# Kernel tuning notes

Measured on AMD Instinct MI355X. Metric: run time of the kernel, lower is better.

Reference implementation:

```python
import jax, jax.numpy as jnp
import numpy as np

N, E = 50000, 800000
IN_DIM, H, OUT = 16, 256, 64
L = 3
REL_DIM, ROLE_DIM, COL_DIM = 16, 8, 8
NUM_REL, NUM_ROLE, NUM_COL = 8, 8, 3
EDGE_IN = 2 * H + REL_DIM + 2 * ROLE_DIM + 2 * COL_DIM   # 560
NODE_IN = 2 * H + ROLE_DIM + COL_DIM                     # 528
LN_EPS = 1e-5


def setup_inputs() -> dict:
    key = jax.random.key(0)
    ks = jax.random.split(key, 32)
    s = 0.02
    inp = {
        "scalars": jax.random.normal(ks[0], (N, IN_DIM), jnp.float32),
        "edge_index": jax.random.randint(ks[1], (2, E), 0, N),
        "edge_relation": jax.random.randint(ks[2], (E,), 0, NUM_REL),
        "node_color_rep": jax.random.randint(ks[3], (N,), 0, NUM_COL),
        "node_role": jax.random.randint(ks[4], (N,), 0, NUM_ROLE),
        # block-level embeddings + input projection (weights stored [in,out])
        "blk_role_emb": jax.random.normal(ks[5], (NUM_ROLE, 8), jnp.float32) * s,
        "blk_color_emb": jax.random.normal(ks[6], (NUM_COL, 8), jnp.float32) * s,
        "in_w": jax.random.normal(ks[7], (IN_DIM + 16, H), jnp.float32) * s,
        "in_b": jnp.zeros((H,), jnp.float32),
        # per-layer params, stacked over L
        "rel_embs": jax.random.normal(ks[8], (L, NUM_REL, REL_DIM), jnp.float32) * s,
        "role_embs": jax.random.normal(ks[9], (L, NUM_ROLE, ROLE_DIM), jnp.float32) * s,
        "col_embs": jax.random.normal(ks[10], (L, NUM_COL, COL_DIM), jnp.float32) * s,
        "e1_w": jax.random.normal(ks[11], (L, EDGE_IN, H), jnp.float32) * s,
        "e1_b": jnp.zeros((L, H), jnp.float32),
        "e2_w": jax.random.normal(ks[12], (L, H, H), jnp.float32) * s,
        "e2_b": jnp.zeros((L, H), jnp.float32),
        "n1_w": jax.random.normal(ks[13], (L, NODE_IN, H), jnp.float32) * s,
        "n1_b": jnp.zeros((L, H), jnp.float32),
        "n2_w": jax.random.normal(ks[14], (L, H, H), jnp.float32) * s,
        "n2_b": jnp.zeros((L, H), jnp.float32),
        "ln_g": jnp.ones((L, H), jnp.float32),
        "ln_b": jnp.zeros((L, H), jnp.float32),
        "out_w": jax.random.normal(ks[15], (H, OUT), jnp.float32) * s,
        "out_b": jnp.zeros((OUT,), jnp.float32),
    }
    return inp


def _layer(h, edge_index, edge_relation, node_color_rep, node_role,
           rel_e, role_e, col_e, e1w, e1b, e2w, e2b, n1w, n1b, n2w, n2b, g, b):
    src, dst = edge_index[0], edge_index[1]
    role_all = role_e[node_role]           # [N, ROLE_DIM]
    col_all = col_e[node_color_rep]        # [N, COL_DIM]
    edge_in = jnp.concatenate(
        [h[src], h[dst], rel_e[edge_relation],
         role_all[src], role_all[dst], col_all[src], col_all[dst]], axis=-1)
    m = jax.nn.silu(edge_in @ e1w + e1b)
    m = jax.nn.silu(m @ e2w + e2b)                       # [E, H]
    agg = jax.ops.segment_sum(m, dst, num_segments=h.shape[0])
    node_in = jnp.concatenate([h, agg, role_all, col_all], axis=-1)
    upd = jax.nn.silu(node_in @ n1w + n1b) @ n2w + n2b
    x = h + upd
    mu = jnp.mean(x, axis=-1, keepdims=True)
    var = jnp.mean(jnp.square(x - mu), axis=-1, keepdims=True)
    return g * (x - mu) * jax.lax.rsqrt(var + LN_EPS) + b


def reference(scalars, edge_index, edge_relation, node_color_rep, node_role,
              blk_role_emb, blk_color_emb, in_w, in_b,
              rel_embs, role_embs, col_embs,
              e1_w, e1_b, e2_w, e2_b, n1_w, n1_b, n2_w, n2_b,
              ln_g, ln_b, out_w, out_b):
    node_in = jnp.concatenate(
        [scalars, blk_color_emb[node_color_rep], blk_role_emb[node_role]], axis=-1)
    h = node_in @ in_w + in_b
    for i in range(L):
        h = _layer(h, edge_index, edge_relation, node_color_rep, node_role,
                   rel_embs[i], role_embs[i], col_embs[i],
                   e1_w[i], e1_b[i], e2_w[i], e2_b[i],
                   n1_w[i], n1_b[i], n2_w[i], n2_b[i],
                   ln_g[i], ln_b[i])
    return h @ out_w + out_b
```

## Files before the change

### kernel.cpp

```cpp
#include <hip/hip_runtime.h>

#define NN 50000
#define NE 800000
#define H 256
#define NB 12500
#define NBINS 50176

typedef __bf16 bf16x8 __attribute__((ext_vector_type(8)));
typedef __bf16 bf16x4 __attribute__((ext_vector_type(4)));
typedef float f32x4 __attribute__((ext_vector_type(4)));

static __device__ __forceinline__ f32x4 mfma16(bf16x8 a, bf16x8 b, f32x4 c) {
  return __builtin_amdgcn_mfma_f32_16x16x32_bf16(a, b, c, 0, 0, 0);
}
static __device__ __forceinline__ bf16x8 bzero8() {
  bf16x8 z;
#pragma unroll
  for (int j = 0; j < 8; ++j) z[j] = (__bf16)0.f;
  return z;
}
static __device__ __forceinline__ float silu_f(float v) {
  return v * __builtin_amdgcn_rcpf(1.f + __builtin_amdgcn_exp2f(v * -1.442695041f));
}
static __device__ __forceinline__ void add4(float4& a, const float4 b) {
  a.x += b.x; a.y += b.y; a.z += b.z; a.w += b.w;
}

__global__ void preph_kernel(
    const float* __restrict__ e1w, const float* __restrict__ e2w,
    const float* __restrict__ n1w, const float* __restrict__ n2w,
    const float* __restrict__ outw, const float* __restrict__ e1b,
    const float* __restrict__ n1b,
    const float* __restrict__ rel_embs, const float* __restrict__ role_embs,
    const float* __restrict__ col_embs, const int* __restrict__ dstI,
    __bf16* __restrict__ wsd, __bf16* __restrict__ e2p,
    __bf16* __restrict__ n1p, __bf16* __restrict__ n2p,
    __bf16* __restrict__ outp, int* __restrict__ cnt,
    float* __restrict__ TR, float* __restrict__ TS, float* __restrict__ TD,
    float* __restrict__ TN)
{
  if (blockIdx.x >= 4675) {
    const int e = (blockIdx.x - 4675) * 256 + threadIdx.x;
    if (e < NE) atomicAdd(&cnt[dstI[e]], 1);
    return;
  }
  int i = blockIdx.x * 256 + threadIdx.x;
  if (i < 3 * 131072) {
    const int l = i / 131072, rem = i % 131072;
    const int c = rem >> 14, r2 = rem & 16383;
    const int n = r2 >> 5, k = c * 32 + (r2 & 31);
    wsd[i] = (n < 256) ? (__bf16)e1w[((size_t)l * 560 + k) * 256 + n]
                       : (__bf16)e1w[((size_t)l * 560 + 256 + k) * 256 + (n - 256)];
    return;
  }
  i -= 3 * 131072;
  if (i < 3 * 65536) {
    const int l = i / 65536, rem = i % 65536;
    const int c = rem >> 13, r2 = rem & 8191;
    const int n = r2 >> 5, k = c * 32 + (r2 & 31);
    e2p[i] = (__bf16)e2w[((size_t)l * 256 + k) * 256 + n];
    return;
  }
  i -= 3 * 65536;
  if (i < 3 * 131072) {
    const int l = i / 131072, rem = i % 131072;
    const int c = rem >> 13, r2 = rem & 8191;
    const int n = r2 >> 5, k = c * 32 + (r2 & 31);
    n1p[i] = (__bf16)n1w[((size_t)l * 528 + k) * 256 + n];
    return;
  }
  i -= 3 * 131072;
  if (i < 3 * 65536) {
    const int l = i / 65536, rem = i % 65536;
    const int c = rem >> 13, r2 = rem & 8191;
    const int n = r2 >> 5, k = c * 32 + (r2 & 31);
    n2p[i] = (__bf16)n2w[((size_t)l * 256 + k) * 256 + n];
    return;
  }
  i -= 3 * 65536;
  if (i < 16384) {
    const int c = i >> 11, r2 = i & 2047;
    const int n = r2 >> 5, k = c * 32 + (r2 & 31);
    outp[i] = (__bf16)outw[(size_t)k * 64 + n];
    return;
  }
  i -= 16384;
  if (i < 768) {
    const int l = i >> 8, c = i & 255;
    float w[48];
#pragma unroll
    for (int j = 0; j < 48; ++j) w[j] = e1w[((size_t)l * 560 + 512 + j) * 256 + c];
#pragma unroll
    for (int r = 0; r < 8; ++r) {
      float s = 0.f;
#pragma unroll
      for (int j = 0; j < 16; ++j) s += rel_embs[l * 128 + r * 16 + j] * w[j];
      TR[((size_t)l * 8 + r) * 256 + c] = s;
    }
    float wn[16];
#pragma unroll
    for (int j = 0; j < 16; ++j) wn[j] = n1w[((size_t)l * 528 + 512 + j) * 256 + c];
    const float bias = e1b[l * 256 + c];
    const float nbias = n1b[l * 256 + c];
#pragma unroll
    for (int ro = 0; ro < 8; ++ro) {
      float ss = 0.f, sd = 0.f, sn = 0.f;
#pragma unroll
      for (int j = 0; j < 8; ++j) {
        const float re = role_embs[l * 64 + ro * 8 + j];
        ss += re * w[16 + j];
        sd += re * w[24 + j];
        sn += re * wn[j];
      }
#pragma unroll
      for (int co = 0; co < 3; ++co) {
        float cs = 0.f, cd = 0.f, cn = 0.f;
#pragma unroll
        for (int j = 0; j < 8; ++j) {
          const float ce = col_embs[l * 24 + co * 8 + j];
          cs += ce * w[32 + j];
          cd += ce * w[40 + j];
          cn += ce * wn[8 + j];
        }
        const size_t o = ((size_t)l * 24 + ro * 3 + co) * 256 + c;
        TS[o] = ss + cs;
        TD[o] = sd + cd + bias;
        TN[o] = sn + cn + nbias;
      }
    }
  }
}

__global__ __launch_bounds__(1024) void scan_kernel(int* __restrict__ cnt) {
  __shared__ int wsum[16];
  __shared__ int carry;
  const int tid = threadIdx.x, lane = tid & 63, wid = tid >> 6;
  if (tid == 0) carry = 0;
  __syncthreads();
  for (int base = 0; base < NBINS; base += 4096) {
    const int idx = base + tid * 4;
    int4 v = make_int4(0, 0, 0, 0);
    if (idx < NBINS) v = *(const int4*)&cnt[idx];
    const int s1 = v.x + v.y, s2 = s1 + v.z, tot = s2 + v.w;
    int x = tot;
#pragma unroll
    for (int d = 1; d < 64; d <<= 1) {
      const int y = __shfl_up(x, d, 64);
      if (lane >= d) x += y;
    }
    if (lane == 63) wsum[wid] = x;
    __syncthreads();
    int wpref = 0;
#pragma unroll
    for (int w = 0; w < 16; ++w)
      if (w < wid) wpref += wsum[w];
    const int ex = carry + wpref + (x - tot);
    if (idx < NBINS) {
      int4 o;
      o.x = ex; o.y = ex + v.x; o.z = ex + s1; o.w = ex + s2;
      *(int4*)&cnt[idx] = o;
    }
    __syncthreads();
    if (tid == 0) {
      int s = 0;
#pragma unroll
      for (int w = 0; w < 16; ++w) s += wsum[w];
      carry += s;
    }
    __syncthreads();
  }
}

__global__ __launch_bounds__(256, 4) void scem_kernel(
    const int* __restrict__ srcI, const int* __restrict__ dstI,
    const int* __restrict__ erel, int* __restrict__ cnt,
    int* __restrict__ esr, int* __restrict__ dstS,
    const float* __restrict__ scalars, const int* __restrict__ ncol,
    const int* __restrict__ nrole,
    const float* __restrict__ colEmb, const float* __restrict__ roleEmb,
    const float* __restrict__ inw, const float* __restrict__ inb,
    const __bf16* __restrict__ wsd,
    const float* __restrict__ TS, const float* __restrict__ TD,
    __bf16* __restrict__ h, __bf16* __restrict__ PS, __bf16* __restrict__ PD)
{
  if (blockIdx.x < 3125) {
    const int e = blockIdx.x * 256 + threadIdx.x;
    if (e < NE) {
      const int d = dstI[e];
      const int pos = atomicAdd(&cnt[d], 1);
      esr[pos] = srcI[e] | (erel[e] << 16);
      dstS[pos] = d;
    }
    return;
  }
  __shared__ __align__(16) char uni[34816];
  __shared__ int sTi[64];
  auto Ain = (__bf16 (*)[40])uni;
  auto Hs  = (__bf16 (*)[264])uni;

  const int tid  = threadIdx.x;
  const int lane = tid & 63;
  const int wave = tid >> 6;
  const int l15  = lane & 15;
  const int quad = lane >> 4;
  const int n0   = (blockIdx.x - 3125) * 64;
  const int colW = wave * 64;

  if (tid < 64) {
    const int n = n0 + tid;
    sTi[tid] = (n < NN) ? (nrole[n] * 3 + ncol[n]) * 256 : 0;
  }
  {
    const int row = tid >> 2, q = tid & 3;
    const int n = n0 + row;
    __bf16* dp = &Ain[row][q * 8];
    if (n < NN) {
      if (q < 2) {
#pragma unroll
        for (int j = 0; j < 8; ++j) dp[j] = (__bf16)scalars[(size_t)n * 16 + q * 8 + j];
      } else if (q == 2) {
        const int c = ncol[n];
#pragma unroll
        for (int j = 0; j < 8; ++j) dp[j] = (__bf16)colEmb[c * 8 + j];
      } else {
        const int r = nrole[n];
#pragma unroll
        for (int j = 0; j < 8; ++j) dp[j] = (__bf16)roleEmb[r * 8 + j];
      }
    } else {
#pragma unroll
      for (int j = 0; j < 8; ++j) dp[j] = (__bf16)0.f;
    }
  }
  __syncthreads();

  f32x4 acc[4][4] = {};
  {
    bf16x8 bfr[4], afr[4];
#pragma unroll
    for (int nj = 0; nj < 4; ++nj) {
      const int col = colW + nj * 16 + l15;
#pragma unroll
      for (int j = 0; j < 8; ++j) bfr[nj][j] = (__bf16)inw[(quad * 8 + j) * 256 + col];
    }
#pragma unroll
    for (int mi = 0; mi < 4; ++mi)
      afr[mi] = *(const bf16x8*)&Ain[mi * 16 + l15][quad * 8];
#pragma unroll
    for (int mi = 0; mi < 4; ++mi)
#pragma unroll
      for (int nj = 0; nj < 4; ++nj)
        acc[mi][nj] = mfma16(afr[mi], bfr[nj], acc[mi][nj]);
  }
  float bi[4];
#pragma unroll
  for (int nj = 0; nj < 4; ++nj) bi[nj] = inb[colW + nj * 16 + l15];
  __syncthreads();

#pragma unroll
  for (int mi = 0; mi < 4; ++mi)
#pragma unroll
    for (int r = 0; r < 4; ++r) {
      const int row = mi * 16 + quad * 4 + r;
      const int n = n0 + row;
#pragma unroll
      for (int nj = 0; nj < 4; ++nj) {
        const int col = colW + nj * 16 + l15;
        const __bf16 hv = (__bf16)(acc[mi][nj][r] + bi[nj]);
        Hs[row][col] = hv;
        if (n < NN) h[(size_t)n * H + col] = hv;
      }
    }
  __syncthreads();

  for (int hf = 0; hf < 2; ++hf) {
    f32x4 ap[4][4] = {};
#pragma unroll
    for (int c = 0; c < 8; ++c) {
      bf16x8 bfr[4], afr[4];
#pragma unroll
      for (int nj = 0; nj < 4; ++nj)
        bfr[nj] = *(const bf16x8*)(wsd + ((size_t)c * 512 + hf * 256 + colW + nj * 16 + l15) * 32 + quad * 8);
#pragma unroll
      for (int mi = 0; mi < 4; ++mi)
        afr[mi] = *(const bf16x8*)&Hs[mi * 16 + l15][c * 32 + quad * 8];
#pragma unroll
      for (int mi = 0; mi < 4; ++mi)
#pragma unroll
        for (int nj = 0; nj < 4; ++nj)
          ap[mi][nj] = mfma16(afr[mi], bfr[nj], ap[mi][nj]);
    }
    const float* T = hf ? TD : TS;
    __bf16* P = hf ? PD : PS;
#pragma unroll
    for (int mi = 0; mi < 4; ++mi)
#pragma unroll
      for (int r = 0; r < 4; ++r) {
        const int row = mi * 16 + quad * 4 + r;
        const int n = n0 + row;
        if (n < NN) {
          const int ti = sTi[row];
#pragma unroll
          for (int nj = 0; nj < 4; ++nj) {
            const int col = colW + nj * 16 + l15;
            P[(size_t)n * H + col] = (__bf16)(ap[mi][nj][r] + T[ti + col]);
          }
        }
      }
  }
}

__global__ __launch_bounds__(256, 4) void edge_kernel(
    const __bf16* __restrict__ PS, const __bf16* __restrict__ PD,
    float* __restrict__ agg, float* __restrict__ bnd,
    const int* __restrict__ esr, const int* __restrict__ dstS,
    const float* __restrict__ TR,
    const __bf16* __restrict__ e2p, const float* __restrict__ e2b)
{
  const int g = blockIdx.x;
  const int bb = (g & 7) * 1563 + (g >> 3);
  if (bb >= NB) return;

  __shared__ __align__(16) char uni[34816];
  __shared__ __bf16 sTrel[8][256];
  __shared__ int sSrc[64], sDst[64], sRel[64];

  auto A2  = (__bf16 (*)[264])uni;
  auto A2t = (__bf16 (*)[68])uni;

  const int tid  = threadIdx.x;
  const int lane = tid & 63;
  const int wave = tid >> 6;
  const int l15  = lane & 15;
  const int quad = lane >> 4;
  const int e0   = bb * 64;
  const int colW = wave * 64;

  if (tid < 64) {
    const int u = esr[e0 + tid];
    sSrc[tid] = u & 0xffff;
    sRel[tid] = u >> 16;
    sDst[tid] = dstS[e0 + tid];
  }
  {
    const int r = tid >> 5, cs = (tid & 31) * 8;
    const float* p = TR + r * 256 + cs;
    bf16x8 v;
#pragma unroll
    for (int j = 0; j < 8; ++j) v[j] = (__bf16)p[j];
    *(bf16x8*)&sTrel[r][cs] = v;
  }
  __syncthreads();

  {
    const int brow = tid >> 5;
    const int cs = (tid & 31) * 8;
#pragma unroll
    for (int it = 0; it < 8; ++it) {
      const int row = it * 8 + brow;
      const bf16x8 a = *(const bf16x8*)(PS + (size_t)sSrc[row] * H + cs);
      const bf16x8 b = *(const bf16x8*)(PD + (size_t)sDst[row] * H + cs);
      const bf16x8 t = *(const bf16x8*)&sTrel[sRel[row]][cs];
      bf16x8 o;
#pragma unroll
      for (int j = 0; j < 8; ++j)
        o[j] = (__bf16)silu_f((float)a[j] + (float)b[j] + (float)t[j]);
      *(bf16x8*)&A2[row][cs] = o;
    }
  }
  __syncthreads();

  f32x4 acc2[4][4] = {};
#pragma unroll
  for (int c = 0; c < 8; ++c) {
    bf16x8 bfr[4], afr[4];
#pragma unroll
    for (int nj = 0; nj < 4; ++nj)
      bfr[nj] = *(const bf16x8*)(e2p + ((size_t)c * 256 + colW + nj * 16 + l15) * 32 + quad * 8);
#pragma unroll
    for (int mi = 0; mi < 4; ++mi)
      afr[mi] = *(const bf16x8*)&A2[mi * 16 + l15][c * 32 + quad * 8];
#pragma unroll
    for (int mi = 0; mi < 4; ++mi)
#pragma unroll
      for (int nj = 0; nj < 4; ++nj)
        acc2[mi][nj] = mfma16(afr[mi], bfr[nj], acc2[mi][nj]);
  }

  float b2[4];
#pragma unroll
  for (int nj = 0; nj < 4; ++nj) b2[nj] = e2b[colW + nj * 16 + l15];
  __syncthreads();

#pragma unroll
  for (int mi = 0; mi < 4; ++mi)
#pragma unroll
    for (int nj = 0; nj < 4; ++nj) {
      const int col = colW + nj * 16 + l15;
      bf16x4 pv;
#pragma unroll
      for (int r = 0; r < 4; ++r)
        pv[r] = (__bf16)silu_f(acc2[mi][nj][r] + b2[nj]);
      *(bf16x4*)&A2t[col][mi * 16 + quad * 4] = pv;
    }
  __syncthreads();

  {
    const int col = tid;
    const bool f = (lane > 0) && (sDst[lane] != sDst[lane - 1]);
    const unsigned long long mask = __ballot(f);
    bf16x4 v[16];
#pragma unroll
    for (int j = 0; j < 16; ++j) v[j] = *(const bf16x4*)&A2t[col][j * 4];
    float* bnd0 = bnd + ((size_t)2 * bb) * 256 + col;
    float sum = 0.f;
    int s0 = 0;
#pragma unroll
    for (int r = 0; r < 64; ++r) {
      sum += (float)v[r >> 2][r & 3];
      if (r == 63 || ((mask >> (r + 1)) & 1ull)) {
        const bool isFirst = (s0 == 0), isLast = (r == 63);
        if (isFirst) {
          bnd0[0] = isLast ? 0.f : sum;
          if (isLast) bnd0[256] = sum;
        } else if (isLast) {
          bnd0[256] = sum;
        } else {
          agg[(size_t)sDst[r] * H + col] = sum;
        }
        sum = 0.f;
        s0 = r + 1;
      }
    }
  }
}

__global__ __launch_bounds__(256, 4) void node_kernel(
    __bf16* __restrict__ h, const float* __restrict__ agg,
    const float* __restrict__ bnd, const int* __restrict__ cnt,
    const int* __restrict__ nrole, const int* __restrict__ ncol,
    const __bf16* __restrict__ n1p, const float* __restrict__ TN,
    const __bf16* __restrict__ n2p, const float* __restrict__ n2b,
    const float* __restrict__ lng, const float* __restrict__ lnb,
    const int mode,
    const __bf16* __restrict__ wsdN, const float* __restrict__ TSn,
    const float* __restrict__ TDn, __bf16* __restrict__ PS, __bf16* __restrict__ PD,
    const __bf16* __restrict__ outp, const float* __restrict__ outb,
    float* __restrict__ out)
{
  __shared__ __align__(16) char uni[33792];
  __shared__ float sSum[64][4], sSsq[64][4];
  __shared__ int sTi[64], sPcnt[64], sPidx[64][4];

  auto Abuf = (__bf16 (*)[72])uni;
  auto A2   = (__bf16 (*)[264])uni;

  const int tid  = threadIdx.x;
  const int lane = tid & 63;
  const int wave = tid >> 6;
  const int l15  = lane & 15;
  const int quad = lane >> 4;
  const int n0   = blockIdx.x * 64;
  const int colW = wave * 64;

  if (tid < 64) {
    const int n = n0 + tid;
    int st = 0, en = 0, ti = 0;
    if (n < NN) {
      st = (n > 0) ? cnt[n - 1] : 0;
      en = cnt[n];
      ti = (nrole[n] * 3 + ncol[n]) * 256;
    }
    sTi[tid] = ti;
    int pc = 0, pidx[4] = {0, 0, 0, 0};
    if (en > st) {
      const int bs = st >> 6, be = (en - 1) >> 6;
      if (bs == be && (st & 63) != 0 && (en & 63) != 0) {
        pc = -1;
      } else {
        for (int b = bs; b <= be && pc < 4; ++b) {
          if (b > bs || (st & 63) == 0) pidx[pc++] = 2 * b;
          if ((b < be || (en & 63) == 0) && pc < 4) pidx[pc++] = 2 * b + 1;
        }
      }
    }
    sPcnt[tid] = pc;
#pragma unroll
    for (int j = 0; j < 4; ++j) sPidx[tid][j] = pidx[j];
  }
  __syncthreads();

  f32x4 acc[4][4] = {};
  for (int s = 0; s < 8; ++s) {
    if (s) __syncthreads();
    if (s < 4) {
#pragma unroll
      for (int it = 0; it < 2; ++it) {
        const int t = tid + it * 256;
        const int row = t >> 3, seg = t & 7;
        const int n = n0 + row;
        bf16x8 v = bzero8();
        if (n < NN) v = *(const bf16x8*)(h + (size_t)n * H + s * 64 + seg * 8);
        *(bf16x8*)&Abuf[row][seg * 8] = v;
      }
    } else {
#pragma unroll
      for (int it = 0; it < 2; ++it) {
        const int t = tid + it * 256;
        const int row = t >> 3, seg = t & 7;
        const int off = (s - 4) * 64 + seg * 8;
        const int pc = sPcnt[row];
        float4 u0 = make_float4(0.f, 0.f, 0.f, 0.f);
        float4 u1 = make_float4(0.f, 0.f, 0.f, 0.f);
        if (pc == -1) {
          const float* p = agg + (size_t)(n0 + row) * H + off;
          u0 = *(const float4*)p;
          u1 = *(const float4*)(p + 4);
        } else {
          for (int j = 0; j < pc; ++j) {
            const float* p = bnd + (size_t)sPidx[row][j] * 256 + off;
            add4(u0, *(const float4*)p);
            add4(u1, *(const float4*)(p + 4));
          }
        }
        bf16x8 v;
        v[0] = (__bf16)u0.x; v[1] = (__bf16)u0.y; v[2] = (__bf16)u0.z; v[3] = (__bf16)u0.w;
        v[4] = (__bf16)u1.x; v[5] = (__bf16)u1.y; v[6] = (__bf16)u1.z; v[7] = (__bf16)u1.w;
        *(bf16x8*)&Abuf[row][seg * 8] = v;
      }
    }
    __syncthreads();
#pragma unroll
    for (int cc = 0; cc < 2; ++cc) {
      const int c = 2 * s + cc;
      bf16x8 bfr[4], afr[4];
#pragma unroll
      for (int nj = 0; nj < 4; ++nj)
        bfr[nj] = *(const bf16x8*)(n1p + ((size_t)c * 256 + colW + nj * 16 + l15) * 32 + quad * 8);
#pragma unroll
      for (int mi = 0; mi < 4; ++mi)
        afr[mi] = *(const bf16x8*)&Abuf[mi * 16 + l15][cc * 32 + quad * 8];
#pragma unroll
      for (int mi = 0; mi < 4; ++mi)
#pragma unroll
        for (int nj = 0; nj < 4; ++nj)
          acc[mi][nj] = mfma16(afr[mi], bfr[nj], acc[mi][nj]);
    }
  }
  __syncthreads();

#pragma unroll
  for (int mi = 0; mi < 4; ++mi)
#pragma unroll
    for (int r = 0; r < 4; ++r) {
      const int row = mi * 16 + quad * 4 + r;
      const int ti = sTi[row];
#pragma unroll
      for (int nj = 0; nj < 4; ++nj) {
        const int col = colW + nj * 16 + l15;
        A2[row][col] = (__bf16)silu_f(acc[mi][nj][r] + TN[ti + col]);
      }
    }
  __syncthreads();

  f32x4 acc2[4][4] = {};
#pragma unroll
  for (int c = 0; c < 8; ++c) {
    bf16x8 bfr[4], afr[4];
#pragma unroll
    for (int nj = 0; nj < 4; ++nj)
      bfr[nj] = *(const bf16x8*)(n2p + ((size_t)c * 256 + colW + nj * 16 + l15) * 32 + quad * 8);
#pragma unroll
    for (int mi = 0; mi < 4; ++mi)
      afr[mi] = *(const bf16x8*)&A2[mi * 16 + l15][c * 32 + quad * 8];
#pragma unroll
    for (int mi = 0; mi < 4; ++mi)
#pragma unroll
      for (int nj = 0; nj < 4; ++nj)
        acc2[mi][nj] = mfma16(afr[mi], bfr[nj], acc2[mi][nj]);
  }

  float b2[4], g4[4], bb4[4];
#pragma unroll
  for (int nj = 0; nj < 4; ++nj) {
    const int col = colW + nj * 16 + l15;
    b2[nj] = n2b[col]; g4[nj] = lng[col]; bb4[nj] = lnb[col];
  }
#pragma unroll
  for (int mi = 0; mi < 4; ++mi)
#pragma unroll
    for (int r = 0; r < 4; ++r) {
      const int n = n0 + mi * 16 + quad * 4 + r;
#pragma unroll
      for (int nj = 0; nj < 4; ++nj) {
        const float hv = (n < NN) ? (float)h[(size_t)n * H + colW + nj * 16 + l15] : 0.f;
        acc2[mi][nj][r] += b2[nj] + hv;
      }
    }
#pragma unroll
  for (int mi = 0; mi < 4; ++mi)
#pragma unroll
    for (int r = 0; r < 4; ++r) {
      float s1 = 0.f, s2 = 0.f;
#pragma unroll
      for (int nj = 0; nj < 4; ++nj) {
        const float v = acc2[mi][nj][r];
        s1 += v; s2 += v * v;
      }
#pragma unroll
      for (int d = 1; d < 16; d <<= 1) {
        s1 += __shfl_xor(s1, d, 16);
        s2 += __shfl_xor(s2, d, 16);
      }
      if (l15 == 0) {
        const int row = mi * 16 + quad * 4 + r;
        sSum[row][wave] = s1; sSsq[row][wave] = s2;
      }
    }
  __syncthreads();

#pragma unroll
  for (int mi = 0; mi < 4; ++mi)
#pragma unroll
    for (int r = 0; r < 4; ++r) {
      const int row = mi * 16 + quad * 4 + r;
      const int n = n0 + row;
      const float t1 = sSum[row][0] + sSum[row][1] + sSum[row][2] + sSum[row][3];
      const float t2 = sSsq[row][0] + sSsq[row][1] + sSsq[row][2] + sSsq[row][3];
      const float mu = t1 * (1.f / 256.f);
      float var = t2 * (1.f / 256.f) - mu * mu;
      var = var < 0.f ? 0.f : var;
      const float rstd = rsqrtf(var + 1e-5f);
#pragma unroll
      for (int nj = 0; nj < 4; ++nj) {
        const int col = colW + nj * 16 + l15;
        const float o = g4[nj] * (acc2[mi][nj][r] - mu) * rstd + bb4[nj];
        const __bf16 ob = (__bf16)o;
        A2[row][col] = ob;
        if (mode == 0 && n < NN) h[(size_t)n * H + col] = ob;
      }
    }
  __syncthreads();

  if (mode == 0) {
    for (int hf = 0; hf < 2; ++hf) {
      f32x4 ap[4][4] = {};
#pragma unroll
      for (int c = 0; c < 8; ++c) {
        bf16x8 bfr[4], afr[4];
#pragma unroll
        for (int nj = 0; nj < 4; ++nj)
          bfr[nj] = *(const bf16x8*)(wsdN + ((size_t)c * 512 + hf * 256 + colW + nj * 16 + l15) * 32 + quad * 8);
#pragma unroll
        for (int mi = 0; mi < 4; ++mi)
          afr[mi] = *(const bf16x8*)&A2[mi * 16 + l15][c * 32 + quad * 8];
#pragma unroll
        for (int mi = 0; mi < 4; ++mi)
#pragma unroll
          for (int nj = 0; nj < 4; ++nj)
            ap[mi][nj] = mfma16(afr[mi], bfr[nj], ap[mi][nj]);
      }
      const float* T = hf ? TDn : TSn;
      __bf16* P = hf ? PD : PS;
#pragma unroll
      for (int mi = 0; mi < 4; ++mi)
#pragma unroll
        for (int r = 0; r < 4; ++r) {
          const int row = mi * 16 + quad * 4 + r;
          const int n = n0 + row;
          if (n < NN) {
            const int ti = sTi[row];
#pragma unroll
            for (int nj = 0; nj < 4; ++nj) {
              const int col = colW + nj * 16 + l15;
              P[(size_t)n * H + col] = (__bf16)(ap[mi][nj][r] + T[ti + col]);
            }
          }
        }
    }
  } else {
    f32x4 ao[4] = {};
#pragma unroll
    for (int c = 0; c < 8; ++c) {
      const bf16x8 bfr = *(const bf16x8*)(outp + ((size_t)c * 64 + wave * 16 + l15) * 32 + quad * 8);
#pragma unroll
      for (int mi = 0; mi < 4; ++mi) {
        const bf16x8 afr = *(const bf16x8*)&A2[mi * 16 + l15][c * 32 + quad * 8];
        ao[mi] = mfma16(afr, bfr, ao[mi]);
      }
    }
    const float ob = outb[wave * 16 + l15];
#pragma unroll
    for (int mi = 0; mi < 4; ++mi)
#pragma unroll
      for (int r = 0; r < 4; ++r) {
        const int n = n0 + mi * 16 + quad * 4 + r;
        if (n < NN) out[(size_t)n * 64 + wave * 16 + l15] = ao[mi][r] + ob;
      }
  }
}

extern "C" void kernel_launch(void* const* d_in, const int* in_sizes, int n_in,
                              void* d_out, int out_size, void* d_ws, size_t ws_size,
                              hipStream_t stream) {
  const float* scalars   = (const float*)d_in[0];
  const int*   ei        = (const int*)d_in[1];
  const int*   erel      = (const int*)d_in[2];
  const int*   ncol      = (const int*)d_in[3];
  const int*   nrole     = (const int*)d_in[4];
  const float* blk_role  = (const float*)d_in[5];
  const float* blk_col   = (const float*)d_in[6];
  const float* inw       = (const float*)d_in[7];
  const float* inb       = (const float*)d_in[8];
  const float* rel_embs  = (const float*)d_in[9];
  const float* role_embs = (const float*)d_in[10];
  const float* col_embs  = (const float*)d_in[11];
  const float* e1w       = (const float*)d_in[12];
  const float* e1b       = (const float*)d_in[13];
  const float* e2w       = (const float*)d_in[14];
  const float* e2b       = (const float*)d_in[15];
  const float* n1w       = (const float*)d_in[16];
  const float* n1b       = (const float*)d_in[17];
  const float* n2w       = (const float*)d_in[18];
  const float* n2b       = (const float*)d_in[19];
  const float* lng       = (const float*)d_in[20];
  const float* lnb       = (const float*)d_in[21];
  const float* outw      = (const float*)d_in[22];
  const float* outb      = (const float*)d_in[23];

  const int* srcI = ei;
  const int* dstI = ei + NE;

  char* ws = (char*)d_ws;
  size_t off = 0;
  auto take = [&](size_t bytes) -> char* {
    off = (off + 255) & ~(size_t)255;
    char* p = ws + off;
    off += bytes;
    return p;
  };
  __bf16* h    = (__bf16*)take((size_t)NN * H * 2);
  float*  agg  = (float*)take((size_t)NN * H * 4);
  float*  bnd  = (float*)take((size_t)2 * NB * 256 * 4);
  __bf16* PS   = (__bf16*)take((size_t)NN * H * 2);
  __bf16* PD   = (__bf16*)take((size_t)NN * H * 2);
  __bf16* wsd  = (__bf16*)take((size_t)3 * 131072 * 2);
  __bf16* e2p  = (__bf16*)take((size_t)3 * 65536 * 2);
  __bf16* n1p  = (__bf16*)take((size_t)3 * 131072 * 2);
  __bf16* n2p  = (__bf16*)take((size_t)3 * 65536 * 2);
  __bf16* outp = (__bf16*)take((size_t)16384 * 2);
  float*  TR   = (float*)take((size_t)3 * 8 * 256 * 4);
  float*  TS   = (float*)take((size_t)3 * 24 * 256 * 4);
  float*  TD   = (float*)take((size_t)3 * 24 * 256 * 4);
  float*  TN   = (float*)take((size_t)3 * 24 * 256 * 4);
  int*    cnt  = (int*)take((size_t)NBINS * 4);
  int*    esr  = (int*)take((size_t)NE * 4);
  int*    dstS = (int*)take((size_t)NE * 4);

  hipMemsetAsync(cnt, 0, (size_t)NBINS * 4, stream);
  preph_kernel<<<7800, 256, 0, stream>>>(
      e1w, e2w, n1w, n2w, outw, e1b, n1b, rel_embs, role_embs, col_embs, dstI,
      wsd, e2p, n1p, n2p, outp, cnt, TR, TS, TD, TN);
  scan_kernel<<<1, 1024, 0, stream>>>(cnt);
  scem_kernel<<<3907, 256, 0, stream>>>(
      srcI, dstI, erel, cnt, esr, dstS,
      scalars, ncol, nrole, blk_col, blk_role, inw, inb,
      wsd, TS, TD, h, PS, PD);

  for (int l = 0; l < 3; ++l) {
    edge_kernel<<<12504, 256, 0, stream>>>(
        PS, PD, agg, bnd, esr, dstS, TR + (size_t)l * 2048,
        e2p + (size_t)l * 65536, e2b + (size_t)l * 256);
    const int mode = (l < 2) ? 0 : 1;
    const int ln = (l + 1 < 3) ? l + 1 : 0;
    node_kernel<<<(NN + 63) / 64, 256, 0, stream>>>(
        h, agg, bnd, cnt, nrole, ncol,
        n1p + (size_t)l * 131072, TN + (size_t)l * 6144,
        n2p + (size_t)l * 65536,  n2b + (size_t)l * 256,
        lng + (size_t)l * 256, lnb + (size_t)l * 256,
        mode,
        wsd + (size_t)ln * 131072, TS + (size_t)ln * 6144, TD + (size_t)ln * 6144,
        PS, PD, outp, outb, (float*)d_out);
  }
}
```

Baseline: 1.348 ms.

## Fold role/color table adds into MFMA via one-hot K-chunk and rework edge sort

Per-node role/color lookup tables (TS/TD/TN) are repacked as bf16 32-wide K chunks, and a one-hot row is appended to the A tile so the table add happens as an extra MFMA step instead of scattered fp32 gathers in the epilogue. The residual h read in node_kernel is replaced by an identity-matrix MFMA that extracts h from the A fragments already in registers. The edge counting sort now stores a permutation and fills dstS from an exclusive prefix copy, with edge_kernel gathering srcI/erel through perm and dropping the block-index swizzle. These trade one more MFMA chunk, extra LDS and lower occupancy (launch bounds 4 to 3) for fewer global gathers, while the edge path gains an indirect load.

```diff
diff --git a/kernel.cpp b/kernel.cpp
--- a/kernel.cpp
+++ b/kernel.cpp
@@ -36,8 +36,8 @@
     __bf16* __restrict__ wsd, __bf16* __restrict__ e2p,
     __bf16* __restrict__ n1p, __bf16* __restrict__ n2p,
     __bf16* __restrict__ outp, int* __restrict__ cnt,
-    float* __restrict__ TR, float* __restrict__ TS, float* __restrict__ TD,
-    float* __restrict__ TN)
+    float* __restrict__ TR, __bf16* __restrict__ TNp,
+    __bf16* __restrict__ TSp, __bf16* __restrict__ TDp)
 {
   if (blockIdx.x >= 4675) {
     const int e = (blockIdx.x - 4675) * 256 + threadIdx.x;
@@ -102,6 +102,7 @@
     for (int j = 0; j < 16; ++j) wn[j] = n1w[((size_t)l * 528 + 512 + j) * 256 + c];
     const float bias = e1b[l * 256 + c];
     const float nbias = n1b[l * 256 + c];
+    const size_t ob = ((size_t)l * 256 + c) * 32;
 #pragma unroll
     for (int ro = 0; ro < 8; ++ro) {
       float ss = 0.f, sd = 0.f, sn = 0.f;
@@ -122,16 +123,23 @@
           cd += ce * w[40 + j];
           cn += ce * wn[8 + j];
         }
-        const size_t o = ((size_t)l * 24 + ro * 3 + co) * 256 + c;
-        TS[o] = ss + cs;
-        TD[o] = sd + cd + bias;
-        TN[o] = sn + cn + nbias;
-      }
-    }
-  }
-}
-
-__global__ __launch_bounds__(1024) void scan_kernel(int* __restrict__ cnt) {
+        const int k = ro * 3 + co;
+        TSp[ob + k] = (__bf16)(ss + cs);
+        TDp[ob + k] = (__bf16)(sd + cd + bias);
+        TNp[ob + k] = (__bf16)(sn + cn + nbias);
+      }
+    }
+#pragma unroll
+    for (int k = 24; k < 32; ++k) {
+      TSp[ob + k] = (__bf16)0.f;
+      TDp[ob + k] = (__bf16)0.f;
+      TNp[ob + k] = (__bf16)0.f;
+    }
+  }
+}
+
+__global__ __launch_bounds__(1024) void scan_kernel(int* __restrict__ cnt,
+                                                    int* __restrict__ cnt2) {
   __shared__ int wsum[16];
   __shared__ int carry;
   const int tid = threadIdx.x, lane = tid & 63, wid = tid >> 6;
@@ -159,6 +167,7 @@
       int4 o;
       o.x = ex; o.y = ex + v.x; o.z = ex + s1; o.w = ex + s2;
       *(int4*)&cnt[idx] = o;
+      *(int4*)&cnt2[idx] = o;
     }
     __syncthreads();
     if (tid == 0) {
@@ -171,44 +180,50 @@
   }
 }
 
-__global__ __launch_bounds__(256, 4) void scem_kernel(
-    const int* __restrict__ srcI, const int* __restrict__ dstI,
-    const int* __restrict__ erel, int* __restrict__ cnt,
-    int* __restrict__ esr, int* __restrict__ dstS,
+__global__ __launch_bounds__(256, 3) void scem_kernel(
+    const int* __restrict__ dstI, int* __restrict__ cnt,
+    const int* __restrict__ cnt2,
+    int* __restrict__ perm, int* __restrict__ dstS,
     const float* __restrict__ scalars, const int* __restrict__ ncol,
     const int* __restrict__ nrole,
     const float* __restrict__ colEmb, const float* __restrict__ roleEmb,
     const float* __restrict__ inw, const float* __restrict__ inb,
     const __bf16* __restrict__ wsd,
-    const float* __restrict__ TS, const float* __restrict__ TD,
+    const __bf16* __restrict__ TSp, const __bf16* __restrict__ TDp,
     __bf16* __restrict__ h, __bf16* __restrict__ PS, __bf16* __restrict__ PD)
 {
-  if (blockIdx.x < 3125) {
-    const int e = blockIdx.x * 256 + threadIdx.x;
+  if (blockIdx.x >= 3907) {
+    const int n = (blockIdx.x - 3907) * 256 + threadIdx.x;
+    if (n < NN) {
+      const int st = cnt2[n], en = cnt2[n + 1];
+      for (int p = st; p < en; ++p) dstS[p] = n;
+    }
+    return;
+  }
+  if (blockIdx.x >= 782) {
+    const int e = (blockIdx.x - 782) * 256 + threadIdx.x;
     if (e < NE) {
-      const int d = dstI[e];
-      const int pos = atomicAdd(&cnt[d], 1);
-      esr[pos] = srcI[e] | (erel[e] << 16);
-      dstS[pos] = d;
+      const int pos = atomicAdd(&cnt[dstI[e]], 1);
+      perm[pos] = e;
     }
     return;
   }
-  __shared__ __align__(16) char uni[34816];
+  __shared__ __align__(16) char uni[37888];
   __shared__ int sTi[64];
   auto Ain = (__bf16 (*)[40])uni;
-  auto Hs  = (__bf16 (*)[264])uni;
+  auto Hs  = (__bf16 (*)[296])uni;
 
   const int tid  = threadIdx.x;
   const int lane = tid & 63;
   const int wave = tid >> 6;
   const int l15  = lane & 15;
   const int quad = lane >> 4;
-  const int n0   = (blockIdx.x - 3125) * 64;
+  const int n0   = blockIdx.x * 64;
   const int colW = wave * 64;
 
   if (tid < 64) {
     const int n = n0 + tid;
-    sTi[tid] = (n < NN) ? (nrole[n] * 3 + ncol[n]) * 256 : 0;
+    sTi[tid] = (n < NN) ? (nrole[n] * 3 + ncol[n]) : 0;
   }
   {
     const int row = tid >> 2, q = tid & 3;
@@ -271,16 +286,27 @@
         if (n < NN) h[(size_t)n * H + col] = hv;
       }
     }
+  {
+    const int row = tid >> 2, q = tid & 3;
+    const int ti = sTi[row];
+    bf16x8 v;
+#pragma unroll
+    for (int j = 0; j < 8; ++j) v[j] = (__bf16)((q * 8 + j == ti) ? 1.f : 0.f);
+    *(bf16x8*)&Hs[row][256 + q * 8] = v;
+  }
   __syncthreads();
 
   for (int hf = 0; hf < 2; ++hf) {
     f32x4 ap[4][4] = {};
 #pragma unroll
-    for (int c = 0; c < 8; ++c) {
+    for (int c = 0; c < 9; ++c) {
       bf16x8 bfr[4], afr[4];
+      const __bf16* bp = (c < 8)
+          ? wsd + ((size_t)c * 512 + hf * 256) * 32
+          : (hf ? TDp : TSp);
 #pragma unroll
       for (int nj = 0; nj < 4; ++nj)
-        bfr[nj] = *(const bf16x8*)(wsd + ((size_t)c * 512 + hf * 256 + colW + nj * 16 + l15) * 32 + quad * 8);
+        bfr[nj] = *(const bf16x8*)(bp + ((size_t)(colW + nj * 16 + l15)) * 32 + quad * 8);
 #pragma unroll
       for (int mi = 0; mi < 4; ++mi)
         afr[mi] = *(const bf16x8*)&Hs[mi * 16 + l15][c * 32 + quad * 8];
@@ -290,7 +316,6 @@
         for (int nj = 0; nj < 4; ++nj)
           ap[mi][nj] = mfma16(afr[mi], bfr[nj], ap[mi][nj]);
     }
-    const float* T = hf ? TD : TS;
     __bf16* P = hf ? PD : PS;
 #pragma unroll
     for (int mi = 0; mi < 4; ++mi)
@@ -299,12 +324,9 @@
         const int row = mi * 16 + quad * 4 + r;
         const int n = n0 + row;
         if (n < NN) {
-          const int ti = sTi[row];
-#pragma unroll
-          for (int nj = 0; nj < 4; ++nj) {
-            const int col = colW + nj * 16 + l15;
-            P[(size_t)n * H + col] = (__bf16)(ap[mi][nj][r] + T[ti + col]);
-          }
+#pragma unroll
+          for (int nj = 0; nj < 4; ++nj)
+            P[(size_t)n * H + colW + nj * 16 + l15] = (__bf16)ap[mi][nj][r];
         }
       }
   }
@@ -313,14 +335,11 @@
 __global__ __launch_bounds__(256, 4) void edge_kernel(
     const __bf16* __restrict__ PS, const __bf16* __restrict__ PD,
     float* __restrict__ agg, float* __restrict__ bnd,
-    const int* __restrict__ esr, const int* __restrict__ dstS,
+    const int* __restrict__ perm, const int* __restrict__ dstS,
+    const int* __restrict__ srcI, const int* __restrict__ erel,
     const float* __restrict__ TR,
     const __bf16* __restrict__ e2p, const float* __restrict__ e2b)
 {
-  const int g = blockIdx.x;
-  const int bb = (g & 7) * 1563 + (g >> 3);
-  if (bb >= NB) return;
-
   __shared__ __align__(16) char uni[34816];
   __shared__ __bf16 sTrel[8][256];
   __shared__ int sSrc[64], sDst[64], sRel[64];
@@ -333,13 +352,13 @@
   const int wave = tid >> 6;
   const int l15  = lane & 15;
   const int quad = lane >> 4;
-  const int e0   = bb * 64;
+  const int e0   = blockIdx.x * 64;
   const int colW = wave * 64;
 
   if (tid < 64) {
-    const int u = esr[e0 + tid];
-    sSrc[tid] = u & 0xffff;
-    sRel[tid] = u >> 16;
+    const int p = perm[e0 + tid];
+    sSrc[tid] = srcI[p];
+    sRel[tid] = erel[p];
     sDst[tid] = dstS[e0 + tid];
   }
   {
@@ -412,7 +431,7 @@
     bf16x4 v[16];
 #pragma unroll
     for (int j = 0; j < 16; ++j) v[j] = *(const bf16x4*)&A2t[col][j * 4];
-    float* bnd0 = bnd + ((size_t)2 * bb) * 256 + col;
+    float* bnd0 = bnd + ((size_t)2 * blockIdx.x) * 256 + col;
     float sum = 0.f;
     int s0 = 0;
 #pragma unroll
@@ -435,25 +454,25 @@
   }
 }
 
-__global__ __launch_bounds__(256, 4) void node_kernel(
+__global__ __launch_bounds__(256, 3) void node_kernel(
     __bf16* __restrict__ h, const float* __restrict__ agg,
-    const float* __restrict__ bnd, const int* __restrict__ cnt,
+    const float* __restrict__ bnd, const int* __restrict__ cnt2,
     const int* __restrict__ nrole, const int* __restrict__ ncol,
-    const __bf16* __restrict__ n1p, const float* __restrict__ TN,
+    const __bf16* __restrict__ n1p, const __bf16* __restrict__ TNp,
     const __bf16* __restrict__ n2p, const float* __restrict__ n2b,
     const float* __restrict__ lng, const float* __restrict__ lnb,
     const int mode,
-    const __bf16* __restrict__ wsdN, const float* __restrict__ TSn,
-    const float* __restrict__ TDn, __bf16* __restrict__ PS, __bf16* __restrict__ PD,
+    const __bf16* __restrict__ wsdN, const __bf16* __restrict__ TSpN,
+    const __bf16* __restrict__ TDpN, __bf16* __restrict__ PS, __bf16* __restrict__ PD,
     const __bf16* __restrict__ outp, const float* __restrict__ outb,
     float* __restrict__ out)
 {
-  __shared__ __align__(16) char uni[33792];
+  __shared__ __align__(16) char uni[37888];
   __shared__ float sSum[64][4], sSsq[64][4];
   __shared__ int sTi[64], sPcnt[64], sPidx[64][4];
 
   auto Abuf = (__bf16 (*)[72])uni;
-  auto A2   = (__bf16 (*)[264])uni;
+  auto A2   = (__bf16 (*)[296])uni;
 
   const int tid  = threadIdx.x;
   const int lane = tid & 63;
@@ -467,9 +486,9 @@
     const int n = n0 + tid;
     int st = 0, en = 0, ti = 0;
     if (n < NN) {
-      st = (n > 0) ? cnt[n - 1] : 0;
-      en = cnt[n];
-      ti = (nrole[n] * 3 + ncol[n]) * 256;
+      st = cnt2[n];
+      en = cnt2[n + 1];
+      ti = nrole[n] * 3 + ncol[n];
     }
     sTi[tid] = ti;
     int pc = 0, pidx[4] = {0, 0, 0, 0};
@@ -490,7 +509,15 @@
   }
   __syncthreads();
 
+  bf16x8 ibfr[2];
+#pragma unroll
+  for (int t = 0; t < 2; ++t)
+#pragma unroll
+    for (int j = 0; j < 8; ++j)
+      ibfr[t][j] = (__bf16)((quad * 8 + j == t * 16 + l15) ? 1.f : 0.f);
+
   f32x4 acc[4][4] = {};
+  f32x4 acch[4][4] = {};
   for (int s = 0; s < 8; ++s) {
     if (s) __syncthreads();
     if (s < 4) {
@@ -545,7 +572,38 @@
 #pragma unroll
         for (int nj = 0; nj < 4; ++nj)
           acc[mi][nj] = mfma16(afr[mi], bfr[nj], acc[mi][nj]);
-    }
+      if (s == wave) {
+#pragma unroll
+        for (int t = 0; t < 2; ++t)
+#pragma unroll
+          for (int mi = 0; mi < 4; ++mi)
+            acch[mi][cc * 2 + t] = mfma16(afr[mi], ibfr[t], acch[mi][cc * 2 + t]);
+      }
+    }
+  }
+  __syncthreads();
+  {
+    const int row = tid >> 2, q = tid & 3;
+    const int ti = sTi[row];
+    bf16x8 v;
+#pragma unroll
+    for (int j = 0; j < 8; ++j) v[j] = (__bf16)((q * 8 + j == ti) ? 1.f : 0.f);
+    *(bf16x8*)&Abuf[row][q * 8] = v;
+  }
+  __syncthreads();
+  {
+    bf16x8 bfr[4], afr[4];
+#pragma unroll
+    for (int nj = 0; nj < 4; ++nj)
+      bfr[nj] = *(const bf16x8*)(TNp + ((size_t)(colW + nj * 16 + l15)) * 32 + quad * 8);
+#pragma unroll
+    for (int mi = 0; mi < 4; ++mi)
+      afr[mi] = *(const bf16x8*)&Abuf[mi * 16 + l15][quad * 8];
+#pragma unroll
+    for (int mi = 0; mi < 4; ++mi)
+#pragma unroll
+      for (int nj = 0; nj < 4; ++nj)
+        acc[mi][nj] = mfma16(afr[mi], bfr[nj], acc[mi][nj]);
   }
   __syncthreads();
 
@@ -554,12 +612,9 @@
 #pragma unroll
     for (int r = 0; r < 4; ++r) {
       const int row = mi * 16 + quad * 4 + r;
-      const int ti = sTi[row];
-#pragma unroll
-      for (int nj = 0; nj < 4; ++nj) {
-        const int col = colW + nj * 16 + l15;
-        A2[row][col] = (__bf16)silu_f(acc[mi][nj][r] + TN[ti + col]);
-      }
+#pragma unroll
+      for (int nj = 0; nj < 4; ++nj)
+        A2[row][colW + nj * 16 + l15] = (__bf16)silu_f(acc[mi][nj][r]);
     }
   __syncthreads();
 
@@ -589,14 +644,11 @@
 #pragma unroll
   for (int mi = 0; mi < 4; ++mi)
 #pragma unroll
-    for (int r = 0; r < 4; ++r) {
-      const int n = n0 + mi * 16 + quad * 4 + r;
-#pragma unroll
-      for (int nj = 0; nj < 4; ++nj) {
-        const float hv = (n < NN) ? (float)h[(size_t)n * H + colW + nj * 16 + l15] : 0.f;
-        acc2[mi][nj][r] += b2[nj] + hv;
-      }
-    }
+    for (int nj = 0; nj < 4; ++nj)
+#pragma unroll
+      for (int r = 0; r < 4; ++r)
+        acc2[mi][nj][r] += b2[nj] + acch[mi][nj][r];
+
 #pragma unroll
   for (int mi = 0; mi < 4; ++mi)
 #pragma unroll
@@ -640,17 +692,28 @@
         if (mode == 0 && n < NN) h[(size_t)n * H + col] = ob;
       }
     }
+  if (mode == 0) {
+    const int row = tid >> 2, q = tid & 3;
+    const int ti = sTi[row];
+    bf16x8 v;
+#pragma unroll
+    for (int j = 0; j < 8; ++j) v[j] = (__bf16)((q * 8 + j == ti) ? 1.f : 0.f);
+    *(bf16x8*)&A2[row][256 + q * 8] = v;
+  }
   __syncthreads();
 
   if (mode == 0) {
     for (int hf = 0; hf < 2; ++hf) {
       f32x4 ap[4][4] = {};
 #pragma unroll
-      for (int c = 0; c < 8; ++c) {
+      for (int c = 0; c < 9; ++c) {
         bf16x8 bfr[4], afr[4];
+        const __bf16* bp = (c < 8)
+            ? wsdN + ((size_t)c * 512 + hf * 256) * 32
+            : (hf ? TDpN : TSpN);
 #pragma unroll
         for (int nj = 0; nj < 4; ++nj)
-          bfr[nj] = *(const bf16x8*)(wsdN + ((size_t)c * 512 + hf * 256 + colW + nj * 16 + l15) * 32 + quad * 8);
+          bfr[nj] = *(const bf16x8*)(bp + ((size_t)(colW + nj * 16 + l15)) * 32 + quad * 8);
 #pragma unroll
         for (int mi = 0; mi < 4; ++mi)
           afr[mi] = *(const bf16x8*)&A2[mi * 16 + l15][c * 32 + quad * 8];
@@ -660,7 +723,6 @@
           for (int nj = 0; nj < 4; ++nj)
             ap[mi][nj] = mfma16(afr[mi], bfr[nj], ap[mi][nj]);
       }
-      const float* T = hf ? TDn : TSn;
       __bf16* P = hf ? PD : PS;
 #pragma unroll
       for (int mi = 0; mi < 4; ++mi)
@@ -669,12 +731,9 @@
           const int row = mi * 16 + quad * 4 + r;
           const int n = n0 + row;
           if (n < NN) {
-            const int ti = sTi[row];
-#pragma unroll
-            for (int nj = 0; nj < 4; ++nj) {
-              const int col = colW + nj * 16 + l15;
-              P[(size_t)n * H + col] = (__bf16)(ap[mi][nj][r] + T[ti + col]);
-            }
+#pragma unroll
+            for (int nj = 0; nj < 4; ++nj)
+              P[(size_t)n * H + colW + nj * 16 + l15] = (__bf16)ap[mi][nj][r];
           }
         }
     }
@@ -750,36 +809,37 @@
   __bf16* n2p  = (__bf16*)take((size_t)3 * 65536 * 2);
   __bf16* outp = (__bf16*)take((size_t)16384 * 2);
   float*  TR   = (float*)take((size_t)3 * 8 * 256 * 4);
-  float*  TS   = (float*)take((size_t)3 * 24 * 256 * 4);
-  float*  TD   = (float*)take((size_t)3 * 24 * 256 * 4);
-  float*  TN   = (float*)take((size_t)3 * 24 * 256 * 4);
+  __bf16* TNp  = (__bf16*)take((size_t)3 * 8192 * 2);
+  __bf16* TSp  = (__bf16*)take((size_t)3 * 8192 * 2);
+  __bf16* TDp  = (__bf16*)take((size_t)3 * 8192 * 2);
   int*    cnt  = (int*)take((size_t)NBINS * 4);
-  int*    esr  = (int*)take((size_t)NE * 4);
+  int*    cnt2 = (int*)take((size_t)NBINS * 4);
+  int*    perm = (int*)take((size_t)NE * 4);
   int*    dstS = (int*)take((size_t)NE * 4);
 
   hipMemsetAsync(cnt, 0, (size_t)NBINS * 4, stream);
   preph_kernel<<<7800, 256, 0, stream>>>(
       e1w, e2w, n1w, n2w, outw, e1b, n1b, rel_embs, role_embs, col_embs, dstI,
-      wsd, e2p, n1p, n2p, outp, cnt, TR, TS, TD, TN);
-  scan_kernel<<<1, 1024, 0, stream>>>(cnt);
-  scem_kernel<<<3907, 256, 0, stream>>>(
-      srcI, dstI, erel, cnt, esr, dstS,
+      wsd, e2p, n1p, n2p, outp, cnt, TR, TNp, TSp, TDp);
+  scan_kernel<<<1, 1024, 0, stream>>>(cnt, cnt2);
+  scem_kernel<<<4103, 256, 0, stream>>>(
+      dstI, cnt, cnt2, perm, dstS,
       scalars, ncol, nrole, blk_col, blk_role, inw, inb,
-      wsd, TS, TD, h, PS, PD);
+      wsd, TSp, TDp, h, PS, PD);
 
   for (int l = 0; l < 3; ++l) {
-    edge_kernel<<<12504, 256, 0, stream>>>(
-        PS, PD, agg, bnd, esr, dstS, TR + (size_t)l * 2048,
+    edge_kernel<<<NB, 256, 0, stream>>>(
+        PS, PD, agg, bnd, perm, dstS, srcI, erel, TR + (size_t)l * 2048,
         e2p + (size_t)l * 65536, e2b + (size_t)l * 256);
     const int mode = (l < 2) ? 0 : 1;
     const int ln = (l + 1 < 3) ? l + 1 : 0;
     node_kernel<<<(NN + 63) / 64, 256, 0, stream>>>(
-        h, agg, bnd, cnt, nrole, ncol,
-        n1p + (size_t)l * 131072, TN + (size_t)l * 6144,
+        h, agg, bnd, cnt2, nrole, ncol,
+        n1p + (size_t)l * 131072, TNp + (size_t)l * 8192,
         n2p + (size_t)l * 65536,  n2b + (size_t)l * 256,
         lng + (size_t)l * 256, lnb + (size_t)l * 256,
         mode,
-        wsd + (size_t)ln * 131072, TS + (size_t)ln * 6144, TD + (size_t)ln * 6144,
+        wsd + (size_t)ln * 131072, TSp + (size_t)ln * 8192, TDp + (size_t)ln * 8192,
         PS, PD, outp, outb, (float*)d_out);
   }
 }
```

Result: slower. 1.453 ms (+7.8%).
